# Kernel optimization log

Hardware: AMD Instinct MI355X
Metric: run time of the kernel (lower is better)

Reference implementation:

```python
import jax, jax.numpy as jnp
import numpy as np
from jax import lax

# 4D convolution via lax.conv_general_dilated (supports N spatial dims natively)
# Layout: x is (N, C, T, U, V, W); weight is (O, I, kT, kU, kV, kW)

def conv4d(x, w, b):
    dn = lax.conv_dimension_numbers(x.shape, w.shape, ('NCTUVW', 'OITUVW', 'NCTUVW'))
    y = lax.conv_general_dilated(x, w, window_strides=(1, 1, 1, 1), padding='SAME',
                                 dimension_numbers=dn)
    return y + b[None, :, None, None, None, None]


def setup_inputs() -> dict:
    key = jax.random.key(0)
    k0, k1, k2, k3, k4 = jax.random.split(key, 5)
    B, C_in, C_hid, C_out = 2, 64, 128, 64
    T, D, H, W = 4, 16, 32, 32
    K = 3  # kernel size per dim (stmode 'C' -> (3,3,3,3))
    x = jax.random.normal(k0, (B, C_in, T, D, H, W), dtype=jnp.float32)
    scale1 = 1.0 / np.sqrt(C_in * K ** 4)
    scale2 = 1.0 / np.sqrt(C_hid * K ** 4)
    w1 = jax.random.normal(k1, (C_hid, C_in, K, K, K, K), dtype=jnp.float32) * scale1
    b1 = jax.random.normal(k2, (C_hid,), dtype=jnp.float32) * scale1
    w2 = jax.random.normal(k3, (C_out, C_hid, K, K, K, K), dtype=jnp.float32) * scale2
    b2 = jax.random.normal(k4, (C_out,), dtype=jnp.float32) * scale2
    return {"x": x, "w1": w1, "b1": b1, "w2": w2, "b2": b2}


def reference(x, w1, b1, w2, b2):
    # conv1 -> ReLU -> (dropout p=0 is identity) -> conv2 -> (dropout identity)
    h = jax.nn.relu(conv4d(x, w1, b1))
    return conv4d(h, w2, b2)
```

## Files before the change

kernel.cpp:

```cpp
#include <hip/hip_runtime.h>


using bf16x8 = __attribute__((ext_vector_type(8))) __bf16;
using f32x16 = __attribute__((ext_vector_type(16))) float;
using f32x4  = __attribute__((ext_vector_type(4))) float;

typedef __attribute__((address_space(1))) const void as1_void;
typedef __attribute__((address_space(3))) void as3_void;
__device__ __forceinline__ void gload_lds16(const void* g, void* l) {
    __builtin_amdgcn_global_load_lds((as1_void*)g, (as3_void*)l, 16, 0, 0);
}

__global__ __launch_bounds__(256) void cvt_x(const float* __restrict__ x,
                                             __bf16* __restrict__ x_t) {
    __shared__ float lt[64][65];
    const int nb = blockIdx.y;
    const int p0 = blockIdx.x * 64;
    const int tu = p0 >> 10;
    const float* src = x + (size_t)nb * 64 * 65536;
    __bf16* dst = x_t + (size_t)nb * 65536 * 64;
    #pragma unroll
    for (int i = 0; i < 16; ++i) {
        int idx = i * 256 + threadIdx.x;
        int c = idx >> 6, p = idx & 63;
        lt[c][p] = src[(size_t)c * 65536 + p0 + p];
    }
    __syncthreads();
    #pragma unroll
    for (int i = 0; i < 16; ++i) {
        int idx = i * 256 + threadIdx.x;
        int c = idx >> 6, pl = idx & 63;
        int p = p0 + pl;
        int v = (p >> 5) & 31, w = p & 31;
        dst[(size_t)(tu * 32 + v) * 2048 + (c >> 3) * 256 + w * 8 + (c & 7)] =
            (__bf16)lt[c][pl];
    }
}

template <int CIN>
__global__ __launch_bounds__(256) void cvt_w(const float* __restrict__ w,
                                             __bf16* __restrict__ wt) {
    constexpr int COUT = 8192 / CIN;
    constexpr int LOGC = (CIN == 64) ? 7 : 6;
    const int tap = blockIdx.x;
    __bf16* dst = wt + (size_t)tap * 8192;
    #pragma unroll
    for (int it = 0; it < 32; ++it) {
        const int i  = it * 256 + threadIdx.x;
        const int cl = i & 15;
        const int o  = (i >> 4) & (COUT - 1);
        const int kg = i >> (4 + LOGC);
        dst[i] = (__bf16)w[(size_t)(o * CIN + kg * 16 + cl) * 81 + tap];
    }
}

template <int CIN, int COUT, int GM, int GN, int WPEU, bool RELU>
__global__ __launch_bounds__(256, WPEU) void conv4d_mfma(
    const __bf16* __restrict__ in_t,
    const __bf16* __restrict__ wt,
    const float* __restrict__ bias,
    __bf16* __restrict__ out_bf,
    float* __restrict__ out_f)
{
    constexpr int KST   = CIN / 16;
    constexpr int UNITS = CIN / 32;
    constexpr int LOGU  = (UNITS == 2) ? 1 : 2;
    constexpr int VSPAN = GM * 4;
    constexpr int VGB   = (VSPAN == 4) ? 3 : 2;
    constexpr int ROWS  = VSPAN + 2;
    constexpr int SLOTS = ROWS * 136;
    constexpr int RNDS  = (SLOTS + 255) / 256;
    constexpr int BUFB  = SLOTS * 16;

    __shared__ __bf16 tile[2 * SLOTS * 8];

    const int tid  = threadIdx.x;
    const int lane = tid & 63;
    const int l31  = lane & 31;
    const int hl   = lane >> 5;
    const int wv   = tid >> 6;
    const int gmi  = (GM == 2) ? (wv >> 1) : 0;
    const int gni  = (GM == 2) ? (wv & 1) : wv;

    const int bid = blockIdx.x;
    const int xcd = bid & 7;
    const int s0  = bid >> 3;
    const int u   = xcd * 2 + (s0 & 1);
    const int vg  = (s0 >> 1) & ((1 << VGB) - 1);
    const int t   = (s0 >> (1 + VGB)) & 3;
    const int nb  = (s0 >> (3 + VGB)) & 1;
    const int v0  = vg * VSPAN;
    const int pbase = ((t * 16 + u) * 32 + v0) * 32;

    const __bf16* inb = in_t + (size_t)nb * 65536 * CIN;

    int goff[RNDS];
    #pragma unroll
    for (int r = 0; r < RNDS; ++r) {
        const int slot = r * 256 + tid;
        const int row  = slot / 136;
        const int rem  = slot - row * 136;
        const int chunk = rem / 34;
        const int wp   = rem - chunk * 34;
        const int v_in = v0 - 1 + row;
        const int w_in = wp - 1;
        const bool ok = (slot < SLOTS) && ((unsigned)v_in < 32u) &&
                        ((unsigned)w_in < 32u);
        goff[r] = ok ? (v_in * (CIN * 32) + chunk * 256 + w_in * 8) : -1;
    }

    #pragma unroll
    for (int r = 0; r < RNDS; ++r) {
        const int slot = r * 256 + tid;
        if (slot < SLOTS && goff[r] < 0) {
            *(uint4*)((char*)tile + slot * 16) = make_uint4(0u, 0u, 0u, 0u);
            *(uint4*)((char*)tile + BUFB + slot * 16) = make_uint4(0u, 0u, 0u, 0u);
        }
    }

    const int lane_base = gmi * 4 * 136 + hl * 34 + l31;
    const bf16x8* tile16 = (const bf16x8*)tile;

    const __bf16* wlane = wt + ((size_t)(gni * 32 + l31)) * 16 + hl * 8;

    int sb[9], tb0[9], nst = 0;
    #pragma unroll
    for (int kt = 0; kt < 3; ++kt) {
        const int t_in = t + kt - 1;
        if ((unsigned)t_in >= 4u) continue;
        #pragma unroll
        for (int ku = 0; ku < 3; ++ku) {
            const int u_in = u + ku - 1;
            if ((unsigned)u_in >= 16u) continue;
            sb[nst]  = (t_in * 16 + u_in) * 1024 * CIN;
            tb0[nst] = (kt * 3 + ku) * 9;
            ++nst;
        }
    }
    const int U = nst * UNITS;

    f32x16 acc[4];
    #pragma unroll
    for (int mt = 0; mt < 4; ++mt)
        #pragma unroll
        for (int i = 0; i < 16; ++i)
            acc[mt][i] = 0.f;

    auto issue = [&](int j) {
        const int st = j >> LOGU, ch = j & (UNITS - 1);
        const __bf16* gb = inb + sb[st] + ch * 1024;
        char* lb = ((char*)tile) + (j & 1) * BUFB + wv * 1024;
        #pragma unroll
        for (int r = 0; r < RNDS; ++r)
            if (goff[r] >= 0)
                gload_lds16(gb + goff[r], lb + r * 4096);
    };

    issue(0);
    #pragma unroll 1
    for (int i = 0; i < U; ++i) {
        asm volatile("s_waitcnt vmcnt(0) lgkmcnt(0)" ::: "memory");
        __syncthreads();
        if (i + 1 < U) issue(i + 1);

        const int st = i >> LOGU, ch = i & (UNITS - 1);
        const int tapb = tb0[st];
        const bf16x8* tb = tile16 + (i & 1) * SLOTS + lane_base;
        #pragma unroll
        for (int ks = 0; ks < 2; ++ks) {
            const int ksg = ch * 2 + ks;
            #pragma unroll
            for (int kw = 0; kw < 3; ++kw) {
                bf16x8 af[6];
                #pragma unroll
                for (int j = 0; j < 6; ++j)
                    af[j] = tb[j * 136 + ks * 68 + kw];
                bf16x8 bv[3];
                #pragma unroll
                for (int kv = 0; kv < 3; ++kv) {
                    const int wo = ((tapb + kv * 3 + kw) * KST + ksg) * (COUT * 16);
                    bv[kv] = *(const bf16x8*)(wlane + wo);
                }
                #pragma unroll
                for (int kv = 0; kv < 3; ++kv)
                    #pragma unroll
                    for (int rr = 0; rr < 4; ++rr)
                        acc[rr] = __builtin_amdgcn_mfma_f32_32x32x16_bf16(
                            af[rr + kv], bv[kv], acc[rr], 0, 0, 0);
            }
        }
    }

    {
        const int o = gni * 32 + l31;
        const float bvls = bias[o];
        #pragma unroll
        for (int rr = 0; rr < 4; ++rr) {
            const int pb = pbase + (gmi * 4 + rr) * 32;
            if constexpr (RELU) {
                #pragma unroll
                for (int rg = 0; rg < 4; ++rg)
                    #pragma unroll
                    for (int j = 0; j < 4; ++j) {
                        float v = acc[rr][rg * 4 + j] + bvls;
                        v = v > 0.f ? v : 0.f;
                        const int p = pb + j + 8 * rg + 4 * hl;
                        const int vv = (p >> 5) & 31, ww = p & 31, tu = p >> 10;
                        out_bf[(size_t)nb * 65536 * COUT +
                               (size_t)(tu * 32 + vv) * (32 * COUT) +
                               (o >> 3) * 256 + ww * 8 + (o & 7)] = (__bf16)v;
                    }
            } else {
                #pragma unroll
                for (int rg = 0; rg < 4; ++rg) {
                    f32x4 sv;
                    #pragma unroll
                    for (int j = 0; j < 4; ++j)
                        sv[j] = acc[rr][rg * 4 + j] + bvls;
                    const int p = pb + 8 * rg + 4 * hl;
                    *(f32x4*)(out_f + ((size_t)nb * COUT + o) * 65536 + p) = sv;
                }
            }
        }
    }
}

extern "C" void kernel_launch(void* const* d_in, const int* in_sizes, int n_in,
                              void* d_out, int out_size, void* d_ws, size_t ws_size,
                              hipStream_t stream) {
    const float* x  = (const float*)d_in[0];
    const float* w1 = (const float*)d_in[1];
    const float* b1 = (const float*)d_in[2];
    const float* w2 = (const float*)d_in[3];
    const float* b2 = (const float*)d_in[4];
    float* out = (float*)d_out;

    char* ws = (char*)d_ws;
    __bf16* x_t = (__bf16*)ws;
    __bf16* h_t = (__bf16*)(ws + 16777216);
    __bf16* w1t = (__bf16*)(ws + 50331648);
    __bf16* w2t = (__bf16*)(ws + 51658752);

    cvt_x<<<dim3(1024, 2), 256, 0, stream>>>(x, x_t);
    cvt_w<64><<<81, 256, 0, stream>>>(w1, w1t);
    cvt_w<128><<<81, 256, 0, stream>>>(w2, w2t);

    conv4d_mfma<64, 128, 1, 4, 3, true><<<1024, 256, 0, stream>>>(x_t, w1t, b1, h_t,
                                                                  nullptr);
    conv4d_mfma<128, 64, 2, 2, 2, false><<<512, 256, 0, stream>>>(h_t, w2t, b2,
                                                                  nullptr, out);
}
```

Before: 386.6 us.

## Software-pipeline LDS/weight loads with MFMAs and vectorize cvt_x stores

The main loop of the MFMA conv kernel now uses double-buffered register fragments. A and B operands for the next (ks,kw) step are loaded while the current 12 MFMAs run, and the first weight fragment of the next unit is prefetched across the barrier. The next async global→LDS issue moves later, into the middle of the compute, and s_setprio is raised around the MFMA groups. cvt_x now writes packed 8-element bf16 vectors instead of scalar stores, and one template parameter of conv1 changes from 3 to 2. Together these aim to hide load latency, at the cost of higher register pressure.

Result: slower. 396.5 us (+2.6%).

```diff
diff --git a/kernel.cpp b/kernel.cpp
--- a/kernel.cpp
+++ b/kernel.cpp
@@ -27,13 +27,17 @@
     }
     __syncthreads();
     #pragma unroll
-    for (int i = 0; i < 16; ++i) {
-        int idx = i * 256 + threadIdx.x;
-        int c = idx >> 6, pl = idx & 63;
+    for (int it = 0; it < 2; ++it) {
+        int idx = it * 256 + threadIdx.x;
+        int pl = idx & 63;
+        int chunk = idx >> 6;
         int p = p0 + pl;
         int v = (p >> 5) & 31, w = p & 31;
-        dst[(size_t)(tu * 32 + v) * 2048 + (c >> 3) * 256 + w * 8 + (c & 7)] =
-            (__bf16)lt[c][pl];
+        bf16x8 pk;
+        #pragma unroll
+        for (int e = 0; e < 8; ++e)
+            pk[e] = (__bf16)lt[chunk * 8 + e][pl];
+        *(bf16x8*)(dst + (size_t)(tu * 32 + v) * 2048 + chunk * 256 + w * 8) = pk;
     }
 }
 
@@ -156,39 +160,60 @@
                 gload_lds16(gb + goff[r], lb + r * 4096);
     };
 
+    auto ldA = [&](const bf16x8* tb, int ks, int kw, bf16x8 (&af)[6]) {
+        #pragma unroll
+        for (int j = 0; j < 6; ++j)
+            af[j] = tb[j * 136 + ks * 68 + kw];
+    };
+    auto ldB = [&](int tapb, int ch, int ks, int kw, bf16x8 (&bv)[3]) {
+        const int ksg = ch * 2 + ks;
+        #pragma unroll
+        for (int kv = 0; kv < 3; ++kv) {
+            const int wo = ((tapb + kv * 3 + kw) * KST + ksg) * (COUT * 16);
+            bv[kv] = *(const bf16x8*)(wlane + wo);
+        }
+    };
+    auto mfma12 = [&](bf16x8 (&af)[6], bf16x8 (&bv)[3]) {
+        __builtin_amdgcn_s_setprio(1);
+        #pragma unroll
+        for (int kv = 0; kv < 3; ++kv)
+            #pragma unroll
+            for (int rr = 0; rr < 4; ++rr)
+                acc[rr] = __builtin_amdgcn_mfma_f32_32x32x16_bf16(
+                    af[rr + kv], bv[kv], acc[rr], 0, 0, 0);
+        __builtin_amdgcn_s_setprio(0);
+    };
+
     issue(0);
+    bf16x8 bvP[3];
+    ldB(tb0[0], 0, 0, 0, bvP);
+
     #pragma unroll 1
     for (int i = 0; i < U; ++i) {
         asm volatile("s_waitcnt vmcnt(0) lgkmcnt(0)" ::: "memory");
         __syncthreads();
-        if (i + 1 < U) issue(i + 1);
 
         const int st = i >> LOGU, ch = i & (UNITS - 1);
         const int tapb = tb0[st];
         const bf16x8* tb = tile16 + (i & 1) * SLOTS + lane_base;
-        #pragma unroll
-        for (int ks = 0; ks < 2; ++ks) {
-            const int ksg = ch * 2 + ks;
-            #pragma unroll
-            for (int kw = 0; kw < 3; ++kw) {
-                bf16x8 af[6];
-                #pragma unroll
-                for (int j = 0; j < 6; ++j)
-                    af[j] = tb[j * 136 + ks * 68 + kw];
-                bf16x8 bv[3];
-                #pragma unroll
-                for (int kv = 0; kv < 3; ++kv) {
-                    const int wo = ((tapb + kv * 3 + kw) * KST + ksg) * (COUT * 16);
-                    bv[kv] = *(const bf16x8*)(wlane + wo);
-                }
-                #pragma unroll
-                for (int kv = 0; kv < 3; ++kv)
-                    #pragma unroll
-                    for (int rr = 0; rr < 4; ++rr)
-                        acc[rr] = __builtin_amdgcn_mfma_f32_32x32x16_bf16(
-                            af[rr + kv], bv[kv], acc[rr], 0, 0, 0);
-            }
-        }
+        const bool more = (i + 1 < U);
+
+        bf16x8 afA[6], afB[6], bvX[3], bvY[3];
+        ldA(tb, 0, 0, afA);
+        ldA(tb, 0, 1, afB); ldB(tapb, ch, 0, 1, bvX);
+        mfma12(afA, bvP);
+        ldA(tb, 0, 2, afA); ldB(tapb, ch, 0, 2, bvY);
+        mfma12(afB, bvX);
+        ldA(tb, 1, 0, afB); ldB(tapb, ch, 1, 0, bvX);
+        mfma12(afA, bvY);
+        ldA(tb, 1, 1, afA); ldB(tapb, ch, 1, 1, bvY);
+        if (more) issue(i + 1);
+        mfma12(afB, bvX);
+        ldA(tb, 1, 2, afB); ldB(tapb, ch, 1, 2, bvX);
+        mfma12(afA, bvY);
+        if (more)
+            ldB(tb0[(i + 1) >> LOGU], (i + 1) & (UNITS - 1), 0, 0, bvP);
+        mfma12(afB, bvX);
     }
 
     {
@@ -245,7 +270,7 @@
     cvt_w<64><<<81, 256, 0, stream>>>(w1, w1t);
     cvt_w<128><<<81, 256, 0, stream>>>(w2, w2t);
 
-    conv4d_mfma<64, 128, 1, 4, 3, true><<<1024, 256, 0, stream>>>(x_t, w1t, b1, h_t,
+    conv4d_mfma<64, 128, 1, 4, 2, true><<<1024, 256, 0, stream>>>(x_t, w1t, b1, h_t,
                                                                   nullptr);
     conv4d_mfma<128, 64, 2, 2, 2, false><<<512, 256, 0, stream>>>(h_t, w2t, b2,
                                                                   nullptr, out);
```

## Replace LDS-staged conv tiles with direct global loads in single-wave blocks

Applied to the files above, without the earlier changes.

The conv kernel drops the double-buffered LDS tile filled through global_load_lds and its per-step barriers. Each 64-thread block now loads A fragments straight from global memory, using clamped addresses and zero-masking at the halo edges. The output-channel split moves into the grid (4096 and 2048 single-wave blocks). This removes the shared-memory staging and synchronization, but input rows are now reloaded redundantly per wave and rely on cache hits. The x transpose kernel also packs 8 channels into one 16-byte vector store.

Measured after the change: 494.7 us. +28.0%, slower.

```diff
diff --git a/kernel.cpp b/kernel.cpp
--- a/kernel.cpp
+++ b/kernel.cpp
@@ -4,12 +4,6 @@
 using bf16x8 = __attribute__((ext_vector_type(8))) __bf16;
 using f32x16 = __attribute__((ext_vector_type(16))) float;
 using f32x4  = __attribute__((ext_vector_type(4))) float;
-
-typedef __attribute__((address_space(1))) const void as1_void;
-typedef __attribute__((address_space(3))) void as3_void;
-__device__ __forceinline__ void gload_lds16(const void* g, void* l) {
-    __builtin_amdgcn_global_load_lds((as1_void*)g, (as3_void*)l, 16, 0, 0);
-}
 
 __global__ __launch_bounds__(256) void cvt_x(const float* __restrict__ x,
                                              __bf16* __restrict__ x_t) {
@@ -27,13 +21,17 @@
     }
     __syncthreads();
     #pragma unroll
-    for (int i = 0; i < 16; ++i) {
-        int idx = i * 256 + threadIdx.x;
-        int c = idx >> 6, pl = idx & 63;
+    for (int it = 0; it < 2; ++it) {
+        int idx = it * 256 + threadIdx.x;
+        int pl = idx & 63;
+        int chunk = idx >> 6;
         int p = p0 + pl;
         int v = (p >> 5) & 31, w = p & 31;
-        dst[(size_t)(tu * 32 + v) * 2048 + (c >> 3) * 256 + w * 8 + (c & 7)] =
-            (__bf16)lt[c][pl];
+        bf16x8 pk;
+        #pragma unroll
+        for (int e = 0; e < 8; ++e)
+            pk[e] = (__bf16)lt[chunk * 8 + e][pl];
+        *(bf16x8*)(dst + (size_t)(tu * 32 + v) * 2048 + chunk * 256 + w * 8) = pk;
     }
 }
 
@@ -54,8 +52,8 @@
     }
 }
 
-template <int CIN, int COUT, int GM, int GN, int WPEU, bool RELU>
-__global__ __launch_bounds__(256, WPEU) void conv4d_mfma(
+template <int CIN, int COUT, int NSPL, bool RELU>
+__global__ __launch_bounds__(64, 4) void conv4d_mfma(
     const __bf16* __restrict__ in_t,
     const __bf16* __restrict__ wt,
     const float* __restrict__ bias,
@@ -65,65 +63,49 @@
     constexpr int KST   = CIN / 16;
     constexpr int UNITS = CIN / 32;
     constexpr int LOGU  = (UNITS == 2) ? 1 : 2;
-    constexpr int VSPAN = GM * 4;
-    constexpr int VGB   = (VSPAN == 4) ? 3 : 2;
-    constexpr int ROWS  = VSPAN + 2;
-    constexpr int SLOTS = ROWS * 136;
-    constexpr int RNDS  = (SLOTS + 255) / 256;
-    constexpr int BUFB  = SLOTS * 16;
-
-    __shared__ __bf16 tile[2 * SLOTS * 8];
-
-    const int tid  = threadIdx.x;
-    const int lane = tid & 63;
-    const int l31  = lane & 31;
-    const int hl   = lane >> 5;
-    const int wv   = tid >> 6;
-    const int gmi  = (GM == 2) ? (wv >> 1) : 0;
-    const int gni  = (GM == 2) ? (wv & 1) : wv;
+    constexpr int VROWB = CIN * 64;
+
+    const int tid = threadIdx.x;
+    const int l31 = tid & 31;
+    const int hl  = tid >> 5;
 
     const int bid = blockIdx.x;
     const int xcd = bid & 7;
     const int s0  = bid >> 3;
     const int u   = xcd * 2 + (s0 & 1);
-    const int vg  = (s0 >> 1) & ((1 << VGB) - 1);
-    const int t   = (s0 >> (1 + VGB)) & 3;
-    const int nb  = (s0 >> (3 + VGB)) & 1;
-    const int v0  = vg * VSPAN;
+    const int vg  = (s0 >> 1) & 7;
+    const int t   = (s0 >> 4) & 3;
+    const int nb  = (s0 >> 6) & 1;
+    const int nsp = (s0 >> 7) & (NSPL - 1);
+    const int v0  = vg * 4;
     const int pbase = ((t * 16 + u) * 32 + v0) * 32;
 
-    const __bf16* inb = in_t + (size_t)nb * 65536 * CIN;
-
-    int goff[RNDS];
-    #pragma unroll
-    for (int r = 0; r < RNDS; ++r) {
-        const int slot = r * 256 + tid;
-        const int row  = slot / 136;
-        const int rem  = slot - row * 136;
-        const int chunk = rem / 34;
-        const int wp   = rem - chunk * 34;
-        const int v_in = v0 - 1 + row;
-        const int w_in = wp - 1;
-        const bool ok = (slot < SLOTS) && ((unsigned)v_in < 32u) &&
-                        ((unsigned)w_in < 32u);
-        goff[r] = ok ? (v_in * (CIN * 32) + chunk * 256 + w_in * 8) : -1;
-    }
-
-    #pragma unroll
-    for (int r = 0; r < RNDS; ++r) {
-        const int slot = r * 256 + tid;
-        if (slot < SLOTS && goff[r] < 0) {
-            *(uint4*)((char*)tile + slot * 16) = make_uint4(0u, 0u, 0u, 0u);
-            *(uint4*)((char*)tile + BUFB + slot * 16) = make_uint4(0u, 0u, 0u, 0u);
-        }
-    }
-
-    const int lane_base = gmi * 4 * 136 + hl * 34 + l31;
-    const bf16x8* tile16 = (const bf16x8*)tile;
-
-    const __bf16* wlane = wt + ((size_t)(gni * 32 + l31)) * 16 + hl * 8;
-
-    int sb[9], tb0[9], nst = 0;
+    const char* inb = (const char*)in_t + (size_t)nb * 65536 * CIN * 2;
+
+    int col[3];
+    #pragma unroll
+    for (int kw = 0; kw < 3; ++kw) {
+        int w_in = l31 + kw - 1;
+        w_in = w_in < 0 ? 0 : (w_in > 31 ? 31 : w_in);
+        col[kw] = w_in * 16;
+    }
+    const bool klo = (l31 == 0);
+    const bool khi = (l31 == 31);
+    const bool vok0 = (vg != 0);
+    const bool vok5 = (vg != 7);
+    int rowoff[6];
+    #pragma unroll
+    for (int j = 0; j < 6; ++j) {
+        int v_in = v0 - 1 + j;
+        v_in = v_in < 0 ? 0 : (v_in > 31 ? 31 : v_in);
+        rowoff[j] = v_in * VROWB;
+    }
+
+    const int o = nsp * 32 + l31;
+    const __bf16* wlane = wt + (size_t)o * 16 + hl * 8;
+
+    unsigned long long pack = 0;
+    int nst = 0;
     #pragma unroll
     for (int kt = 0; kt < 3; ++kt) {
         const int t_in = t + kt - 1;
@@ -132,8 +114,7 @@
         for (int ku = 0; ku < 3; ++ku) {
             const int u_in = u + ku - 1;
             if ((unsigned)u_in >= 16u) continue;
-            sb[nst]  = (t_in * 16 + u_in) * 1024 * CIN;
-            tb0[nst] = (kt * 3 + ku) * 9;
+            pack |= (unsigned long long)(kt * 3 + ku) << (4 * nst);
             ++nst;
         }
     }
@@ -146,57 +127,65 @@
         for (int i = 0; i < 16; ++i)
             acc[mt][i] = 0.f;
 
-    auto issue = [&](int j) {
-        const int st = j >> LOGU, ch = j & (UNITS - 1);
-        const __bf16* gb = inb + sb[st] + ch * 1024;
-        char* lb = ((char*)tile) + (j & 1) * BUFB + wv * 1024;
-        #pragma unroll
-        for (int r = 0; r < RNDS; ++r)
-            if (goff[r] >= 0)
-                gload_lds16(gb + goff[r], lb + r * 4096);
-    };
-
-    issue(0);
+    bf16x8 z8;
+    #pragma unroll
+    for (int e = 0; e < 8; ++e) z8[e] = (__bf16)0.0f;
+
     #pragma unroll 1
     for (int i = 0; i < U; ++i) {
-        asm volatile("s_waitcnt vmcnt(0) lgkmcnt(0)" ::: "memory");
-        __syncthreads();
-        if (i + 1 < U) issue(i + 1);
-
-        const int st = i >> LOGU, ch = i & (UNITS - 1);
-        const int tapb = tb0[st];
-        const bf16x8* tb = tile16 + (i & 1) * SLOTS + lane_base;
-        #pragma unroll
-        for (int ks = 0; ks < 2; ++ks) {
+        const int st   = i >> LOGU;
+        const int ch   = i & (UNITS - 1);
+        const int code = (int)((pack >> (st * 4)) & 15);
+        const int kt   = (code * 11) >> 5;
+        const int ku   = code - kt * 3;
+        const int tapb = code * 9;
+        const char* ub = inb +
+            (size_t)(((t + kt - 1) * 16 + (u + ku - 1)) * 1024 * CIN +
+                     ch * 1024) * 2;
+
+        auto group = [&](int ks, int kw, bool maskall) {
             const int ksg = ch * 2 + ks;
-            #pragma unroll
-            for (int kw = 0; kw < 3; ++kw) {
-                bf16x8 af[6];
+            bf16x8 bv[3];
+            #pragma unroll
+            for (int kv = 0; kv < 3; ++kv) {
+                const int wo = ((tapb + kv * 3 + kw) * KST + ksg) * (COUT * 16);
+                bv[kv] = *(const bf16x8*)(wlane + wo);
+            }
+            const int loff = (ks * 2 + hl) * 512 + col[kw];
+            bf16x8 af[6];
+            #pragma unroll
+            for (int j = 0; j < 6; ++j)
+                af[j] = *(const bf16x8*)(ub + rowoff[j] + loff);
+            const bool kl = maskall ? ((kw == 0) ? klo : khi) : false;
+            #pragma unroll
+            for (int j = 0; j < 6; ++j) {
+                bool dead = kl;
+                if (j == 0) dead = dead || !vok0;
+                if (j == 5) dead = dead || !vok5;
+                if (maskall || j == 0 || j == 5)
+                    af[j] = dead ? z8 : af[j];
+            }
+            #pragma unroll
+            for (int kv = 0; kv < 3; ++kv)
                 #pragma unroll
-                for (int j = 0; j < 6; ++j)
-                    af[j] = tb[j * 136 + ks * 68 + kw];
-                bf16x8 bv[3];
-                #pragma unroll
-                for (int kv = 0; kv < 3; ++kv) {
-                    const int wo = ((tapb + kv * 3 + kw) * KST + ksg) * (COUT * 16);
-                    bv[kv] = *(const bf16x8*)(wlane + wo);
-                }
-                #pragma unroll
-                for (int kv = 0; kv < 3; ++kv)
-                    #pragma unroll
-                    for (int rr = 0; rr < 4; ++rr)
-                        acc[rr] = __builtin_amdgcn_mfma_f32_32x32x16_bf16(
-                            af[rr + kv], bv[kv], acc[rr], 0, 0, 0);
-            }
-        }
+                for (int rr = 0; rr < 4; ++rr)
+                    acc[rr] = __builtin_amdgcn_mfma_f32_32x32x16_bf16(
+                        af[rr + kv], bv[kv], acc[rr], 0, 0, 0);
+        };
+
+        group(0, 0, true);
+        group(0, 1, false);
+        group(0, 2, true);
+        group(1, 0, true);
+        group(1, 1, false);
+        group(1, 2, true);
     }
 
     {
-        const int o = gni * 32 + l31;
         const float bvls = bias[o];
         #pragma unroll
         for (int rr = 0; rr < 4; ++rr) {
-            const int pb = pbase + (gmi * 4 + rr) * 32;
+            const int pb = pbase + rr * 32;
             if constexpr (RELU) {
                 #pragma unroll
                 for (int rg = 0; rg < 4; ++rg)
@@ -245,8 +234,8 @@
     cvt_w<64><<<81, 256, 0, stream>>>(w1, w1t);
     cvt_w<128><<<81, 256, 0, stream>>>(w2, w2t);
 
-    conv4d_mfma<64, 128, 1, 4, 3, true><<<1024, 256, 0, stream>>>(x_t, w1t, b1, h_t,
-                                                                  nullptr);
-    conv4d_mfma<128, 64, 2, 2, 2, false><<<512, 256, 0, stream>>>(h_t, w2t, b2,
-                                                                  nullptr, out);
-}
+    conv4d_mfma<64, 128, 4, true><<<4096, 64, 0, stream>>>(x_t, w1t, b1, h_t,
+                                                           nullptr);
+    conv4d_mfma<128, 64, 2, false><<<2048, 64, 0, stream>>>(h_t, w2t, b2,
+                                                            nullptr, out);
+}
```
